# Optimization experiments

Hardware: AMD Instinct MI355X
Metric: run time of the kernel (lower is better)

The kernel has to match this reference:

```python
import jax, jax.numpy as jnp
import numpy as np

EPS = 1e-5
P = 2  # polynomial kernel degree


def setup_inputs() -> dict:
    key = jax.random.key(0)
    k1, k2, k3 = jax.random.split(key, 3)
    b, t, h, d = 2, 2048, 8, 64
    Q = jax.random.normal(k1, (b, t, h, d), jnp.float32)
    K = jax.random.normal(k2, (b, t, h, d), jnp.float32)
    V = jax.random.normal(k3, (b, t, h, d), jnp.float32)
    return {"Q": Q, "K": K, "V": V, "chunk_count": 16}


def reference(Q, K, V, chunk_count):
    b, t, h, d = Q.shape
    dv = V.shape[-1]
    c = chunk_count
    n = t // c  # tokens per chunk

    def to_chunked(X):
        # [b, t, h, d] -> [c, b, h, n, d]
        return X.reshape(b, c, n, h, X.shape[-1]).transpose(1, 0, 3, 2, 4)

    Qc, Kc, Vc = to_chunked(Q), to_chunked(K), to_chunked(V)

    # ---- per-chunk states: s = K^T K, S = sum_n (K_n outer K_n) outer V_n ----
    s_loc = jnp.einsum('cbhni,cbhnj->cbhij', Kc, Kc)                 # [c,b,h,d,d]
    S_loc = jnp.einsum('cbhni,cbhnj,cbhnv->cbhijv', Kc, Kc, Vc)      # [c,b,h,d,d,dv]
    # inclusive cumulative merge over chunks
    S = jnp.cumsum(S_loc, axis=0)
    s = jnp.cumsum(s_loc, axis=0)

    # ---- local within-chunk masked quadratic attention ----
    D = jnp.einsum('cbhqi,cbhki->cbhqk', Qc, Kc)                     # [c,b,h,n,n]
    C = D ** P
    mask = jnp.tril(jnp.ones((n, n), dtype=bool))
    B = jnp.where(mask, C, 0.0)
    Y = jnp.einsum('cbhqk,cbhkv->cbhqv', B, Vc)                      # [c,b,h,n,dv]
    Z = B.sum(-1) + EPS                                              # [c,b,h,n]

    # ---- cross-chunk contribution: chunk i>0 attends to state of chunks <i ----
    Qp = Qc[1:]
    Sp, sp = S[:-1], s[:-1]
    num = jnp.einsum('cbhni,cbhnj,cbhijv->cbhnv', Qp, Qp, Sp)
    den = jnp.einsum('cbhni,cbhnj,cbhij->cbhn', Qp, Qp, sp)
    Y = Y.at[1:].add(num)
    Z = Z.at[1:].add(den)

    out = (Y / Z[..., None]).transpose(1, 0, 3, 2, 4).reshape(b, t, h, dv)
    return out
```

## Files before the change

kernel.cpp:

```cpp
#include <hip/hip_runtime.h>
#include <hip/hip_fp16.h>

typedef __attribute__((ext_vector_type(8))) _Float16 f16x8;
typedef __attribute__((ext_vector_type(4))) _Float16 f16x4;
typedef __attribute__((ext_vector_type(8))) unsigned short u16x8;
typedef __attribute__((ext_vector_type(4))) float f32x4;

constexpr int NT = 256;
constexpr int TILE_SHORTS = 4096;

__device__ __forceinline__ int swzoff(int row, int c) {
    return row * 64 + ((c ^ (row & 7)) << 3);
}
__device__ __forceinline__ unsigned short f2h_u(float x) {
    return __half_as_ushort(__float2half(x));
}

__global__ __launch_bounds__(256, 4) void prepass(
    const float* __restrict__ Kg, const float* __restrict__ Vg,
    unsigned short* __restrict__ Kw, unsigned short* __restrict__ Vw)
{
    __shared__ __align__(16) float Vl[64 * 68];
    const int tile = blockIdx.x;
    const int bh   = blockIdx.y;
    const int b = bh >> 3, h = bh & 7;
    const int tid = threadIdx.x;
    const size_t gbase = (((size_t)b * 2048 + tile * 64) * 8 + h) * 64;

    #pragma unroll
    for (int j = 0; j < 4; ++j) {
        int id = j * 256 + tid, row = id >> 4, c4 = id & 15;
        *(float4*)&Vl[row * 68 + c4 * 4] =
            *(const float4*)&Vg[gbase + (size_t)row * 512 + c4 * 4];
    }

    unsigned short* Ko = Kw + (size_t)(bh * 32 + tile) * TILE_SHORTS;
    #pragma unroll
    for (int j = 0; j < 2; ++j) {
        int id = j * 256 + tid, row = id >> 3, c = id & 7;
        const float* src = &Kg[gbase + (size_t)row * 512 + c * 8];
        float4 x = *(const float4*)src, y = *(const float4*)(src + 4);
        u16x8 o;
        o[0] = f2h_u(x.x); o[1] = f2h_u(x.y); o[2] = f2h_u(x.z); o[3] = f2h_u(x.w);
        o[4] = f2h_u(y.x); o[5] = f2h_u(y.y); o[6] = f2h_u(y.z); o[7] = f2h_u(y.w);
        *(u16x8*)&Ko[swzoff(row, c)] = o;
    }
    __syncthreads();

    unsigned short* Vo = Vw + (size_t)(bh * 32 + tile) * TILE_SHORTS;
    #pragma unroll
    for (int j = 0; j < 2; ++j) {
        int id = j * 256 + tid, vrow = id >> 3, g = id & 7;
        u16x8 o;
        #pragma unroll
        for (int jj = 0; jj < 8; ++jj) {
            int kk = ((g & 1) * 2 + (jj >> 2)) * 16 + (g >> 1) * 4 + (jj & 3);
            o[jj] = f2h_u(Vl[kk * 68 + vrow]);
        }
        *(u16x8*)&Vo[swzoff(vrow, g)] = o;
    }
}

__global__ __launch_bounds__(NT, 2) void attn_pow2_f16(
    const float* __restrict__ Qg,
    const unsigned short* __restrict__ Kw, const unsigned short* __restrict__ Vw,
    float* __restrict__ Og)
{
    const int tid  = threadIdx.x;
    const int lane = tid & 63;
    const int wave = tid >> 6;
    const int a    = lane & 15;
    const int quad = lane >> 4;
    const int m0   = wave * 16;

    int r0 = (int)blockIdx.x;
    int wr = (r0 < 256) ? r0 : (767 - r0);
    const int qt = 31 - (wr >> 4);
    const int bh = wr & 15;
    const int b = bh >> 3, h = bh & 7;
    const int q0 = qt * 64;

    f16x8 bQ[2];
    {
        const size_t qrowbase = (((size_t)b * 2048 + q0 + m0 + a) * 8 + h) * 64;
        #pragma unroll
        for (int ks = 0; ks < 2; ++ks) {
            const float* src = &Qg[qrowbase + ks * 32 + quad * 8];
            float4 x = *(const float4*)src, y = *(const float4*)(src + 4);
            u16x8 o;
            o[0] = f2h_u(x.x); o[1] = f2h_u(x.y); o[2] = f2h_u(x.z); o[3] = f2h_u(x.w);
            o[4] = f2h_u(y.x); o[5] = f2h_u(y.y); o[6] = f2h_u(y.z); o[7] = f2h_u(y.w);
            bQ[ks] = __builtin_bit_cast(f16x8, o);
        }
    }

    const unsigned short* Ktiles = Kw + (size_t)bh * 32 * TILE_SHORTS;
    const unsigned short* Vtiles = Vw + (size_t)bh * 32 * TILE_SHORTS;

    int koff[8], voff[8];
    #pragma unroll
    for (int s = 0; s < 4; ++s) {
        koff[s * 2 + 0] = swzoff(s * 16 + a, quad);
        koff[s * 2 + 1] = swzoff(s * 16 + a, 4 + quad);
        voff[s * 2 + 0] = swzoff(s * 16 + a, quad * 2);
        voff[s * 2 + 1] = swzoff(s * 16 + a, quad * 2 + 1);
    }

    u16x8 c0K[8], c0V[8], c1K[8], c1V[8];
    auto gload = [&](int kt, u16x8 (&rk)[8], u16x8 (&rv)[8]) {
        const unsigned short* kg = Ktiles + (size_t)kt * TILE_SHORTS;
        const unsigned short* vg = Vtiles + (size_t)kt * TILE_SHORTS;
        #pragma unroll
        for (int i = 0; i < 8; ++i) {
            rk[i] = *(const u16x8*)&kg[koff[i]];
            rv[i] = *(const u16x8*)&vg[voff[i]];
        }
    };

    f32x4 oacc[4];
    #pragma unroll
    for (int n = 0; n < 4; ++n) oacc[n] = (f32x4){0.f, 0.f, 0.f, 0.f};
    float den_l = 0.f;

    union U8 { u16x8 u; f16x4 q[2]; f16x8 f; };

    auto compute = [&](const u16x8 (&rk)[8], const u16x8 (&rv)[8], bool diag) {
        f32x4 sacc[4];
        #pragma unroll
        for (int s = 0; s < 4; ++s) sacc[s] = (f32x4){0.f, 0.f, 0.f, 0.f};
        #pragma unroll
        for (int s = 0; s < 4; ++s) {
            #pragma unroll
            for (int ks = 0; ks < 2; ++ks) {
                U8 ak; ak.u = rk[s * 2 + ks];
                sacc[s] = __builtin_amdgcn_mfma_f32_16x16x32_f16(ak.f, bQ[ks], sacc[s], 0, 0, 0);
            }
        }
        f16x4 aS[4];
        #pragma unroll
        for (int s = 0; s < 4; ++s) {
            float p[4];
            #pragma unroll
            for (int r = 0; r < 4; ++r) {
                float d0 = sacc[s][r];
                float v = d0 * d0;
                if (diag && (s * 16 + quad * 4 + r) > (m0 + a)) v = 0.f;
                p[r] = v;
            }
            den_l += (p[0] + p[1]) + (p[2] + p[3]);
            aS[s] = (f16x4){(_Float16)p[0], (_Float16)p[1], (_Float16)p[2], (_Float16)p[3]};
        }
        #pragma unroll
        for (int n = 0; n < 4; ++n) {
            U8 va, vb;
            va.u = rv[n * 2 + 0];
            vb.u = rv[n * 2 + 1];
            oacc[n] = __builtin_amdgcn_mfma_f32_16x16x16f16(aS[0], va.q[0], oacc[n], 0, 0, 0);
            oacc[n] = __builtin_amdgcn_mfma_f32_16x16x16f16(aS[1], va.q[1], oacc[n], 0, 0, 0);
            oacc[n] = __builtin_amdgcn_mfma_f32_16x16x16f16(aS[2], vb.q[0], oacc[n], 0, 0, 0);
            oacc[n] = __builtin_amdgcn_mfma_f32_16x16x16f16(aS[3], vb.q[1], oacc[n], 0, 0, 0);
        }
    };

    gload(0, c0K, c0V);
    for (int kt = 0; kt <= qt; kt += 2) {
        if (kt + 1 <= qt) gload(kt + 1, c1K, c1V);
        compute(c0K, c0V, kt == qt);
        if (kt + 1 <= qt) {
            if (kt + 2 <= qt) gload(kt + 2, c0K, c0V);
            compute(c1K, c1V, kt + 1 == qt);
        }
    }

    den_l += __shfl_xor(den_l, 16);
    den_l += __shfl_xor(den_l, 32);

    float invz[4];
    #pragma unroll
    for (int r = 0; r < 4; ++r) {
        float dq = __shfl(den_l, quad * 4 + r);
        invz[r] = 1.0f / (dq + 1e-5f);
    }

    #pragma unroll
    for (int n = 0; n < 4; ++n) {
        #pragma unroll
        for (int r = 0; r < 4; ++r) {
            int t = q0 + m0 + quad * 4 + r;
            int v = n * 16 + a;
            Og[(((size_t)b * 2048 + t) * 8 + h) * 64 + v] = oacc[n][r] * invz[r];
        }
    }
}

extern "C" void kernel_launch(void* const* d_in, const int* in_sizes, int n_in,
                              void* d_out, int out_size, void* d_ws, size_t ws_size,
                              hipStream_t stream) {
    const float* Q = (const float*)d_in[0];
    const float* K = (const float*)d_in[1];
    const float* V = (const float*)d_in[2];
    float* O = (float*)d_out;
    unsigned short* Kw = (unsigned short*)d_ws;
    unsigned short* Vw = Kw + (size_t)16 * 32 * TILE_SHORTS;

    prepass<<<dim3(32, 16), 256, 0, stream>>>(K, V, Kw, Vw);
    attn_pow2_f16<<<dim3(512), NT, 0, stream>>>(Q, Kw, Vw, O);
}
```

Baseline: 102.4 us.

## Pair causal query tiles per block and split KV tiles across wave groups

Each block now handles two query tiles (qt and 31-qt) so every block gets an equal amount of causal work. Within a block, four groups of two waves split the KV tiles (split-K), staging them through LDS, and each wave covers 32 query rows so every K/V fragment feeds two MFMAs. Partial outputs and denominators are reduced across groups in LDS before the normalized store. The cost is extra barriers, an LDS reduction pass and fewer blocks (256 of 512 threads), which may lower latency hiding.

```diff
diff --git a/kernel.cpp b/kernel.cpp
--- a/kernel.cpp
+++ b/kernel.cpp
@@ -6,7 +6,7 @@
 typedef __attribute__((ext_vector_type(8))) unsigned short u16x8;
 typedef __attribute__((ext_vector_type(4))) float f32x4;
 
-constexpr int NT = 256;
+constexpr int NT = 512;
 constexpr int TILE_SHORTS = 4096;
 
 __device__ __forceinline__ int swzoff(int row, int c) {
@@ -66,129 +66,202 @@
     const unsigned short* __restrict__ Kw, const unsigned short* __restrict__ Vw,
     float* __restrict__ Og)
 {
+    __shared__ __align__(16) unsigned short lds[4 * 2 * TILE_SHORTS];
     const int tid  = threadIdx.x;
     const int lane = tid & 63;
     const int wave = tid >> 6;
+    const int g    = wave >> 1;
+    const int w2   = wave & 1;
     const int a    = lane & 15;
     const int quad = lane >> 4;
-    const int m0   = wave * 16;
-
-    int r0 = (int)blockIdx.x;
-    int wr = (r0 < 256) ? r0 : (767 - r0);
-    const int qt = 31 - (wr >> 4);
-    const int bh = wr & 15;
+    const int gt   = tid & 127;
+
+    const int r0 = (int)blockIdx.x;
+    const int bh = r0 & 15, p = r0 >> 4;
     const int b = bh >> 3, h = bh & 7;
-    const int q0 = qt * 64;
-
-    f16x8 bQ[2];
-    {
-        const size_t qrowbase = (((size_t)b * 2048 + q0 + m0 + a) * 8 + h) * 64;
-        #pragma unroll
-        for (int ks = 0; ks < 2; ++ks) {
-            const float* src = &Qg[qrowbase + ks * 32 + quad * 8];
-            float4 x = *(const float4*)src, y = *(const float4*)(src + 4);
-            u16x8 o;
-            o[0] = f2h_u(x.x); o[1] = f2h_u(x.y); o[2] = f2h_u(x.z); o[3] = f2h_u(x.w);
-            o[4] = f2h_u(y.x); o[5] = f2h_u(y.y); o[6] = f2h_u(y.z); o[7] = f2h_u(y.w);
-            bQ[ks] = __builtin_bit_cast(f16x8, o);
-        }
-    }
+    const int TqA = 31 - p, TqB = p;
+    const int IA = (TqA + 4) >> 2;
 
     const unsigned short* Ktiles = Kw + (size_t)bh * 32 * TILE_SHORTS;
     const unsigned short* Vtiles = Vw + (size_t)bh * 32 * TILE_SHORTS;
-
-    int koff[8], voff[8];
-    #pragma unroll
-    for (int s = 0; s < 4; ++s) {
-        koff[s * 2 + 0] = swzoff(s * 16 + a, quad);
-        koff[s * 2 + 1] = swzoff(s * 16 + a, 4 + quad);
-        voff[s * 2 + 0] = swzoff(s * 16 + a, quad * 2);
-        voff[s * 2 + 1] = swzoff(s * 16 + a, quad * 2 + 1);
-    }
-
-    u16x8 c0K[8], c0V[8], c1K[8], c1V[8];
-    auto gload = [&](int kt, u16x8 (&rk)[8], u16x8 (&rv)[8]) {
-        const unsigned short* kg = Ktiles + (size_t)kt * TILE_SHORTS;
-        const unsigned short* vg = Vtiles + (size_t)kt * TILE_SHORTS;
-        #pragma unroll
-        for (int i = 0; i < 8; ++i) {
-            rk[i] = *(const u16x8*)&kg[koff[i]];
-            rv[i] = *(const u16x8*)&vg[voff[i]];
+    unsigned short* const Kb = lds + g * (2 * TILE_SHORTS);
+    unsigned short* const Vb = Kb + TILE_SHORTS;
+
+    union U8 { u16x8 u; f16x4 q[2]; f16x8 f; };
+
+    f16x8 bQ[2][2];
+    auto loadBQ = [&](int Tq) {
+        #pragma unroll
+        for (int st = 0; st < 2; ++st) {
+            const size_t rowbase =
+                (((size_t)b * 2048 + Tq * 64 + w2 * 32 + st * 16 + a) * 8 + h) * 64;
+            #pragma unroll
+            for (int ks = 0; ks < 2; ++ks) {
+                const float* src = &Qg[rowbase + ks * 32 + quad * 8];
+                float4 x = *(const float4*)src, y = *(const float4*)(src + 4);
+                u16x8 o;
+                o[0] = f2h_u(x.x); o[1] = f2h_u(x.y); o[2] = f2h_u(x.z); o[3] = f2h_u(x.w);
+                o[4] = f2h_u(y.x); o[5] = f2h_u(y.y); o[6] = f2h_u(y.z); o[7] = f2h_u(y.w);
+                bQ[st][ks] = __builtin_bit_cast(f16x8, o);
+            }
         }
     };
-
-    f32x4 oacc[4];
-    #pragma unroll
-    for (int n = 0; n < 4; ++n) oacc[n] = (f32x4){0.f, 0.f, 0.f, 0.f};
-    float den_l = 0.f;
-
-    union U8 { u16x8 u; f16x4 q[2]; f16x8 f; };
-
-    auto compute = [&](const u16x8 (&rk)[8], const u16x8 (&rv)[8], bool diag) {
-        f32x4 sacc[4];
-        #pragma unroll
-        for (int s = 0; s < 4; ++s) sacc[s] = (f32x4){0.f, 0.f, 0.f, 0.f};
-        #pragma unroll
-        for (int s = 0; s < 4; ++s) {
-            #pragma unroll
-            for (int ks = 0; ks < 2; ++ks) {
-                U8 ak; ak.u = rk[s * 2 + ks];
-                sacc[s] = __builtin_amdgcn_mfma_f32_16x16x32_f16(ak.f, bQ[ks], sacc[s], 0, 0, 0);
-            }
-        }
-        f16x4 aS[4];
-        #pragma unroll
-        for (int s = 0; s < 4; ++s) {
-            float p[4];
-            #pragma unroll
-            for (int r = 0; r < 4; ++r) {
-                float d0 = sacc[s][r];
-                float v = d0 * d0;
-                if (diag && (s * 16 + quad * 4 + r) > (m0 + a)) v = 0.f;
-                p[r] = v;
-            }
-            den_l += (p[0] + p[1]) + (p[2] + p[3]);
-            aS[s] = (f16x4){(_Float16)p[0], (_Float16)p[1], (_Float16)p[2], (_Float16)p[3]};
-        }
-        #pragma unroll
-        for (int n = 0; n < 4; ++n) {
-            U8 va, vb;
-            va.u = rv[n * 2 + 0];
-            vb.u = rv[n * 2 + 1];
-            oacc[n] = __builtin_amdgcn_mfma_f32_16x16x16f16(aS[0], va.q[0], oacc[n], 0, 0, 0);
-            oacc[n] = __builtin_amdgcn_mfma_f32_16x16x16f16(aS[1], va.q[1], oacc[n], 0, 0, 0);
-            oacc[n] = __builtin_amdgcn_mfma_f32_16x16x16f16(aS[2], vb.q[0], oacc[n], 0, 0, 0);
-            oacc[n] = __builtin_amdgcn_mfma_f32_16x16x16f16(aS[3], vb.q[1], oacc[n], 0, 0, 0);
-        }
+    loadBQ(TqA);
+
+    u16x8 rK[4], rV[4];
+    auto gload = [&](int kt) {
+        const u16x8* kg = (const u16x8*)(Ktiles + (size_t)kt * TILE_SHORTS);
+        const u16x8* vg = (const u16x8*)(Vtiles + (size_t)kt * TILE_SHORTS);
+        #pragma unroll
+        for (int j = 0; j < 4; ++j) { rK[j] = kg[j * 128 + gt]; rV[j] = vg[j * 128 + gt]; }
     };
-
-    gload(0, c0K, c0V);
-    for (int kt = 0; kt <= qt; kt += 2) {
-        if (kt + 1 <= qt) gload(kt + 1, c1K, c1V);
-        compute(c0K, c0V, kt == qt);
-        if (kt + 1 <= qt) {
-            if (kt + 2 <= qt) gload(kt + 2, c0K, c0V);
-            compute(c1K, c1V, kt + 1 == qt);
-        }
-    }
-
-    den_l += __shfl_xor(den_l, 16);
-    den_l += __shfl_xor(den_l, 32);
-
-    float invz[4];
-    #pragma unroll
-    for (int r = 0; r < 4; ++r) {
-        float dq = __shfl(den_l, quad * 4 + r);
-        invz[r] = 1.0f / (dq + 1e-5f);
-    }
-
-    #pragma unroll
-    for (int n = 0; n < 4; ++n) {
-        #pragma unroll
-        for (int r = 0; r < 4; ++r) {
-            int t = q0 + m0 + quad * 4 + r;
-            int v = n * 16 + a;
-            Og[(((size_t)b * 2048 + t) * 8 + h) * 64 + v] = oacc[n][r] * invz[r];
+    gload(g);
+
+    f32x4 oacc[2][4];
+    #pragma unroll
+    for (int st = 0; st < 2; ++st)
+        #pragma unroll
+        for (int n = 0; n < 4; ++n) oacc[st][n] = (f32x4){0.f, 0.f, 0.f, 0.f};
+    float den[2] = {0.f, 0.f};
+
+    for (int it = 0; it < 9; ++it) {
+        const bool inB = it >= IA;
+        const int  i   = inB ? it - IA : it;
+        const int  Tq  = inB ? TqB : TqA;
+        const int  kt  = i * 4 + g;
+        const bool valid = kt <= Tq;
+
+        if (valid) {
+            u16x8* kd = (u16x8*)Kb; u16x8* vd = (u16x8*)Vb;
+            #pragma unroll
+            for (int j = 0; j < 4; ++j) { kd[j * 128 + gt] = rK[j]; vd[j * 128 + gt] = rV[j]; }
+        }
+        __syncthreads();
+
+        {
+            const int itn = it + 1;
+            if (itn < 9) {
+                const bool inBn = itn >= IA;
+                const int  in_  = inBn ? itn - IA : itn;
+                const int  ktn  = in_ * 4 + g;
+                if (ktn <= (inBn ? TqB : TqA)) gload(ktn);
+            }
+        }
+
+        if (valid) {
+            f32x4 sacc[2][4];
+            #pragma unroll
+            for (int st = 0; st < 2; ++st)
+                #pragma unroll
+                for (int s = 0; s < 4; ++s) sacc[st][s] = (f32x4){0.f, 0.f, 0.f, 0.f};
+            #pragma unroll
+            for (int s = 0; s < 4; ++s) {
+                #pragma unroll
+                for (int ks = 0; ks < 2; ++ks) {
+                    U8 ak; ak.u = *(const u16x8*)&Kb[swzoff(s * 16 + a, ks * 4 + quad)];
+                    #pragma unroll
+                    for (int st = 0; st < 2; ++st)
+                        sacc[st][s] = __builtin_amdgcn_mfma_f32_16x16x32_f16(
+                            ak.f, bQ[st][ks], sacc[st][s], 0, 0, 0);
+                }
+            }
+            const bool diag = (kt == Tq);
+            f16x4 aS[2][4];
+            #pragma unroll
+            for (int st = 0; st < 2; ++st) {
+                const int qrow = w2 * 32 + st * 16 + a;
+                #pragma unroll
+                for (int s = 0; s < 4; ++s) {
+                    float pv[4];
+                    #pragma unroll
+                    for (int r = 0; r < 4; ++r) {
+                        float d0 = sacc[st][s][r];
+                        float v = d0 * d0;
+                        if (diag && (s * 16 + quad * 4 + r) > qrow) v = 0.f;
+                        pv[r] = v;
+                    }
+                    den[st] += (pv[0] + pv[1]) + (pv[2] + pv[3]);
+                    aS[st][s] = (f16x4){(_Float16)pv[0], (_Float16)pv[1],
+                                        (_Float16)pv[2], (_Float16)pv[3]};
+                }
+            }
+            #pragma unroll
+            for (int n = 0; n < 4; ++n) {
+                U8 va, vb_;
+                va.u  = *(const u16x8*)&Vb[swzoff(n * 16 + a, quad * 2)];
+                vb_.u = *(const u16x8*)&Vb[swzoff(n * 16 + a, quad * 2 + 1)];
+                #pragma unroll
+                for (int st = 0; st < 2; ++st) {
+                    oacc[st][n] = __builtin_amdgcn_mfma_f32_16x16x16f16(aS[st][0], va.q[0],  oacc[st][n], 0, 0, 0);
+                    oacc[st][n] = __builtin_amdgcn_mfma_f32_16x16x16f16(aS[st][1], va.q[1],  oacc[st][n], 0, 0, 0);
+                    oacc[st][n] = __builtin_amdgcn_mfma_f32_16x16x16f16(aS[st][2], vb_.q[0], oacc[st][n], 0, 0, 0);
+                    oacc[st][n] = __builtin_amdgcn_mfma_f32_16x16x16f16(aS[st][3], vb_.q[1], oacc[st][n], 0, 0, 0);
+                }
+            }
+        }
+        __syncthreads();
+
+        if (it == IA - 1 || it == 8) {
+            float d0 = den[0], d1 = den[1];
+            d0 += __shfl_xor(d0, 16); d0 += __shfl_xor(d0, 32);
+            d1 += __shfl_xor(d1, 16); d1 += __shfl_xor(d1, 32);
+            float* Op = (float*)lds;
+            float* Dp = (float*)lds + 6 * 32 * 65;
+            if (g > 0) {
+                const int base = ((g - 1) * 2 + w2) * (32 * 65);
+                #pragma unroll
+                for (int st = 0; st < 2; ++st)
+                    #pragma unroll
+                    for (int n = 0; n < 4; ++n)
+                        #pragma unroll
+                        for (int r = 0; r < 4; ++r)
+                            Op[base + (st * 16 + quad * 4 + r) * 65 + n * 16 + a] = oacc[st][n][r];
+            }
+            if (quad == 0) {
+                Dp[((g * 2 + w2) * 2 + 0) * 16 + a] = d0;
+                Dp[((g * 2 + w2) * 2 + 1) * 16 + a] = d1;
+            }
+            __syncthreads();
+            if (g == 0) {
+                #pragma unroll
+                for (int st = 0; st < 2; ++st) {
+                    float invz[4];
+                    #pragma unroll
+                    for (int r = 0; r < 4; ++r) {
+                        float s = 1e-5f;
+                        #pragma unroll
+                        for (int gg = 0; gg < 4; ++gg)
+                            s += Dp[((gg * 2 + w2) * 2 + st) * 16 + quad * 4 + r];
+                        invz[r] = 1.0f / s;
+                    }
+                    #pragma unroll
+                    for (int n = 0; n < 4; ++n) {
+                        f32x4 o = oacc[st][n];
+                        #pragma unroll
+                        for (int gg = 1; gg < 4; ++gg) {
+                            const int base = ((gg - 1) * 2 + w2) * (32 * 65);
+                            #pragma unroll
+                            for (int r = 0; r < 4; ++r)
+                                o[r] += Op[base + (st * 16 + quad * 4 + r) * 65 + n * 16 + a];
+                        }
+                        #pragma unroll
+                        for (int r = 0; r < 4; ++r) {
+                            const int t = Tq * 64 + w2 * 32 + st * 16 + quad * 4 + r;
+                            Og[(((size_t)b * 2048 + t) * 8 + h) * 64 + n * 16 + a] = o[r] * invz[r];
+                        }
+                    }
+                }
+            }
+            __syncthreads();
+            if (it == IA - 1) {
+                #pragma unroll
+                for (int st = 0; st < 2; ++st) {
+                    den[st] = 0.f;
+                    #pragma unroll
+                    for (int n = 0; n < 4; ++n) oacc[st][n] = (f32x4){0.f, 0.f, 0.f, 0.f};
+                }
+                loadBQ(TqB);
+            }
         }
     }
 }
@@ -204,5 +277,5 @@
     unsigned short* Vw = Kw + (size_t)16 * 32 * TILE_SHORTS;
 
     prepass<<<dim3(32, 16), 256, 0, stream>>>(K, V, Kw, Vw);
-    attn_pow2_f16<<<dim3(512), NT, 0, stream>>>(Q, Kw, Vw, O);
-}
+    attn_pow2_f16<<<dim3(256), NT, 0, stream>>>(Q, Kw, Vw, O);
+}
```

Result: faster. 99.73 us (-2.7%).
